# Kernel tuning notes

Measured on AMD Instinct MI355X. Metric: run time of the kernel, lower is better.

## Reference

```python
import jax, jax.numpy as jnp
import numpy as np

H, KV, D, HID = 16, 4, 64, 1024
OUT_MIN, OUT_MAX = 32, 8192  # output_size_max = config.max_position_embeddings


def _score_attn(x, Wq, Wk, Wv, Wo):
    # Full (non-causal, unmasked) GQA attention whose o_proj maps to 1 scalar/token.
    B, S, _ = x.shape
    q = (x @ Wq).reshape(B, S, H, D)
    k = jnp.repeat((x @ Wk).reshape(B, S, KV, D), H // KV, axis=2)  # repeat_kv
    v = jnp.repeat((x @ Wv).reshape(B, S, KV, D), H // KV, axis=2)
    scores = jnp.einsum('bqhd,bkhd->bhqk', q, k) / jnp.asarray(np.sqrt(D), x.dtype)
    a = jax.nn.softmax(scores, axis=-1)
    o = jnp.einsum('bhqk,bkhd->bqhd', a, v).reshape(B, S, H * D)
    return o @ Wo  # (B, S, 1)


def _dynamic_sizes(x, Wq, Wk, Wv, Wo, scale):
    s = _score_attn(x, Wq, Wk, Wv, Wo)               # (B,S,1)
    means = jax.nn.sigmoid(s).mean(axis=1)            # (B,1) (no attention_mask)
    sizes = means.squeeze(-1) * scale * (OUT_MAX - OUT_MIN) + OUT_MIN
    return sizes.astype(jnp.int32)                    # torch .int() truncation


def _segment_ids(sizes_np, S, max_len):
    # torch.linspace(0, L, sz+1).long() boundaries; token t -> segment i with
    # intervals[i] <= t < intervals[i+1]; right-aligned into [max_len] per batch.
    B = len(sizes_np)
    seg = np.zeros((B, S), np.int32)
    t = np.arange(S)
    for b, sz in enumerate(sizes_np):
        sz = int(sz)
        bnd = np.floor(np.linspace(0.0, S, sz + 1, dtype=np.float64)).astype(np.int64)
        s = np.clip(np.searchsorted(bnd, t, side='right') - 1, 0, sz - 1)
        seg[b] = b * max_len + (max_len - sz) + s
    return jnp.asarray(seg)


def setup_inputs() -> dict:
    key = jax.random.key(0)
    ks = jax.random.split(key, 10)
    B, S = 4, 2048
    x = jax.random.normal(ks[0], (B, S, HID), jnp.float32)
    def lin(k, i, o):
        return jax.random.normal(k, (i, o), jnp.float32) / np.sqrt(i).astype(np.float32)
    return dict(
        hidden_states=x,
        Wq1=lin(ks[1], HID, H * D), Wk1=lin(ks[2], HID, KV * D),
        Wv1=lin(ks[3], HID, KV * D), Wo1=lin(ks[4], H * D, 1),
        Wq2=lin(ks[5], HID, H * D), Wk2=lin(ks[6], HID, KV * D),
        Wv2=lin(ks[7], HID, KV * D), Wo2=lin(ks[8], H * D, 1),
        scale_param=jnp.asarray(0.01, jnp.float32),
    )


def reference(hidden_states, Wq1, Wk1, Wv1, Wo1, Wq2, Wk2, Wv2, Wo2, scale_param):
    B, S, Hd = hidden_states.shape
    # 1) size-estimation attention -> per-batch dynamic output sizes (data-dependent shape)
    sizes = _dynamic_sizes(hidden_states, Wq1, Wk1, Wv1, Wo1, scale_param)
    sizes_np = np.asarray(jax.device_get(sizes))
    max_len = int(sizes_np.max())
    seg = _segment_ids(sizes_np, S, max_len)          # (B,S) global segment ids
    # 2) weighted-pooling attention -> per-token sigmoid weights
    w = jax.nn.sigmoid(_score_attn(hidden_states, Wq2, Wk2, Wv2, Wo2)).squeeze(-1)  # (B,S)
    # 3) weighted average pooling over dynamic-size segments (vectorized scatter-add)
    num = jax.ops.segment_sum((hidden_states * w[..., None]).reshape(B * S, Hd),
                              seg.reshape(-1), num_segments=B * max_len)
    den = jax.ops.segment_sum(w.reshape(-1), seg.reshape(-1), num_segments=B * max_len)
    pooled = (num / (den[:, None] + 1e-8)).reshape(B, max_len, Hd)
    out_mask = jnp.arange(max_len)[None, :] >= (max_len - sizes)[:, None]
    return pooled, out_mask, sizes
```

## Files before the change

kernel.cpp:

```cpp
#include <hip/hip_runtime.h>
#include <math.h>

#define TB 256

constexpr int B_ = 4, S_ = 2048, HID_ = 1024, H_ = 16, KV_ = 4, D_ = 64;

typedef short sh8 __attribute__((ext_vector_type(8)));
typedef float fl4 __attribute__((ext_vector_type(4)));
typedef unsigned short u16;
typedef unsigned int u32;

__device__ __forceinline__ u16 f2bf(float f) {
  u32 u = __float_as_uint(f);
  u += 0x7fff + ((u >> 16) & 1);
  return (u16)(u >> 16);
}
__device__ __forceinline__ float bf2f(u16 h) { return __uint_as_float(((u32)h) << 16); }

constexpr size_t XSZ   = (size_t)B_ * S_ * HID_;
constexpr size_t WQH_O = 2 * XSZ;
constexpr size_t WQSZ  = (size_t)2 * HID_ * (H_ * D_);
constexpr size_t WQL_O = WQH_O + WQSZ;
constexpr size_t WKH_O = WQH_O + 2 * WQSZ;
constexpr size_t WKSZ  = (size_t)2 * HID_ * (KV_ * D_);
constexpr size_t WKL_O = WKH_O + WKSZ;
constexpr size_t KH_O  = WKH_O + 2 * WKSZ;
constexpr size_t KSZ   = (size_t)2 * B_ * KV_ * S_ * D_;
constexpr size_t KL_O  = KH_O + KSZ;
constexpr size_t KPLANE = (size_t)S_ * D_;
constexpr size_t FBASE   = (KH_O + 2 * KSZ) / 2;
constexpr size_t U_OFF   = FBASE;
constexpr size_t U_SZ    = (size_t)2 * B_ * H_ * S_;
constexpr size_t WVO_OFF = U_OFF + U_SZ;
constexpr size_t WVO_SZ  = (size_t)HID_ * 32;
constexpr size_t SH_OFF  = WVO_OFF + WVO_SZ;
constexpr size_t SH_SZ   = (size_t)2 * B_ * S_ * H_;
constexpr size_t W_OFF   = SH_OFF + SH_SZ;
constexpr size_t W_SZ    = (size_t)B_ * S_;
constexpr size_t SUM_OFF = W_OFF + W_SZ;

__device__ __forceinline__ void conv_w_body(
    const float* __restrict__ W1, const float* __restrict__ W2,
    u16* __restrict__ OH, u16* __restrict__ OL, int ncols,
    int blk, int tid, float wt[32][257]) {
  int ngrp = ncols >> 8;
  int a = blk / (32 * ngrp);
  int rem = blk - a * 32 * ngrp;
  int cs = rem / ngrp, ng = rem - cs * ngrp;
  const float* W = a ? W2 : W1;
#pragma unroll
  for (int i = 0; i < 8; ++i) {
    int e = tid + i * 256;
    int r = e >> 6, c4 = (e & 63) * 4;
    float4 v = *reinterpret_cast<const float4*>(
        W + ((size_t)(cs * 32 + r)) * ncols + ng * 256 + c4);
    wt[r][c4] = v.x; wt[r][c4 + 1] = v.y; wt[r][c4 + 2] = v.z; wt[r][c4 + 3] = v.w;
  }
  __syncthreads();
  int w = tid >> 6, lane = tid & 63, quad = lane >> 4, col = lane & 15;
  int NF = ncols >> 4;
#pragma unroll
  for (int f = 0; f < 4; ++f) {
    int n16 = w * 4 + f;
    sh8 hh, ll;
#pragma unroll
    for (int j = 0; j < 8; ++j) {
      float v = wt[quad * 8 + j][n16 * 16 + col];
      u16 hb = f2bf(v);
      hh[j] = (short)hb;
      ll[j] = (short)f2bf(v - bf2f(hb));
    }
    size_t fb = (((size_t)a * 32 + cs) * NF + ng * 16 + n16) * 512 + (size_t)lane * 8;
    *reinterpret_cast<sh8*>(OH + fb) = hh;
    *reinterpret_cast<sh8*>(OL + fb) = ll;
  }
}

__global__ __launch_bounds__(TB) void prep1_kernel(
    const float* __restrict__ x,
    const float* __restrict__ Wq1, const float* __restrict__ Wq2,
    const float* __restrict__ Wk1, const float* __restrict__ Wk2,
    const float* __restrict__ Wv1, const float* __restrict__ Wo1,
    const float* __restrict__ Wv2, const float* __restrict__ Wo2,
    float* __restrict__ ws) {
  __shared__ float wt[32][257];
  int blk = blockIdx.x, tid = threadIdx.x;
  u16* wsu = (u16*)ws;
  if (blk < 512) {
    u16* XH = wsu;
    u16* XL = XH + XSZ;
    int bt = blk;
    int w = tid >> 6, lane = tid & 63, quad = lane >> 4, col = lane & 15;
    int b = bt >> 7, t16 = bt & 127;
    const float* row = x + ((size_t)b * S_ + t16 * 16 + col) * HID_;
#pragma unroll
    for (int i = 0; i < 8; ++i) {
      int cs = w + i * 4;
      const float* src = row + cs * 32 + quad * 8;
      float4 v0 = *reinterpret_cast<const float4*>(src);
      float4 v1 = *reinterpret_cast<const float4*>(src + 4);
      float vv[8] = {v0.x, v0.y, v0.z, v0.w, v1.x, v1.y, v1.z, v1.w};
      sh8 hh, ll;
#pragma unroll
      for (int j = 0; j < 8; ++j) {
        u16 hb = f2bf(vv[j]);
        hh[j] = (short)hb;
        ll[j] = (short)f2bf(vv[j] - bf2f(hb));
      }
      size_t fb = ((size_t)bt * 32 + cs) * 512 + (size_t)lane * 8;
      *reinterpret_cast<sh8*>(XH + fb) = hh;
      *reinterpret_cast<sh8*>(XL + fb) = ll;
    }
  } else if (blk < 768) {
    conv_w_body(Wq1, Wq2, wsu + WQH_O, wsu + WQL_O, H_ * D_, blk - 512, tid, wt);
  } else if (blk < 832) {
    conv_w_body(Wk1, Wk2, wsu + WKH_O, wsu + WKL_O, KV_ * D_, blk - 768, tid, wt);
  } else {
    int n = blk - 832, a = n >> 4, h = n & 15, kv = h >> 2;
    const float* Wv = a ? Wv2 : Wv1;
    const float* Wo = a ? Wo2 : Wo1;
    for (int c = tid; c < HID_; c += TB) {
      const float* vr = Wv + (size_t)c * (KV_ * D_) + kv * D_;
      const float* wo = Wo + h * D_;
      float acc = 0.f;
#pragma unroll 16
      for (int d = 0; d < D_; ++d) acc += vr[d] * wo[d];
      ws[WVO_OFF + (size_t)c * 32 + n] = acc;
    }
  }
}

__global__ __launch_bounds__(TB) void prep2_kernel(
    const float* __restrict__ x, float* __restrict__ ws) {
  __shared__ __align__(16) float xs[64][68];
  __shared__ float uw[64][36];
  int blk = blockIdx.x, tid = threadIdx.x;
  if (blk < 1024) {
    int k0 = (blk & 31) * 64;
    int kv = (blk >> 5) & 3;
    int ab = blk >> 7, a = ab >> 2, b = ab & 3;
    int w = tid >> 6, lane = tid & 63, quad = lane >> 4, col = lane & 15;
    const u16* XH = (const u16*)ws;
    const u16* XL = XH + XSZ;
    const u16* WKH = XH + WKH_O;
    const u16* WKL = XH + WKL_O;
    int tq = (w & 1) * 2, nq = (w >> 1) * 2;
    fl4 C[2][2] = {};
#pragma unroll 2
    for (int cs = 0; cs < 32; ++cs) {
      sh8 ah[2], al[2], bh[2], bl[2];
#pragma unroll
      for (int ti = 0; ti < 2; ++ti) {
        size_t fb = (((size_t)b * 128 + (k0 >> 4) + tq + ti) * 32 + cs) * 512 + (size_t)lane * 8;
        ah[ti] = *reinterpret_cast<const sh8*>(XH + fb);
        if (a == 0) al[ti] = *reinterpret_cast<const sh8*>(XL + fb);
      }
#pragma unroll
      for (int ni = 0; ni < 2; ++ni) {
        size_t fb = (((size_t)a * 32 + cs) * 16 + kv * 4 + nq + ni) * 512 + (size_t)lane * 8;
        bh[ni] = *reinterpret_cast<const sh8*>(WKH + fb);
        if (a == 0) bl[ni] = *reinterpret_cast<const sh8*>(WKL + fb);
      }
#pragma unroll
      for (int ti = 0; ti < 2; ++ti)
#pragma unroll
        for (int ni = 0; ni < 2; ++ni) {
          C[ti][ni] = __builtin_amdgcn_mfma_f32_16x16x32_bf16(ah[ti], bh[ni], C[ti][ni], 0, 0, 0);
          if (a == 0) {
            C[ti][ni] = __builtin_amdgcn_mfma_f32_16x16x32_bf16(al[ti], bh[ni], C[ti][ni], 0, 0, 0);
            C[ti][ni] = __builtin_amdgcn_mfma_f32_16x16x32_bf16(ah[ti], bl[ni], C[ti][ni], 0, 0, 0);
          }
        }
    }
#pragma unroll
    for (int ti = 0; ti < 2; ++ti)
#pragma unroll
      for (int ni = 0; ni < 2; ++ni)
#pragma unroll
        for (int r = 0; r < 4; ++r)
          xs[(tq + ti) * 16 + quad * 4 + r][(nq + ni) * 16 + col] = C[ti][ni][r];
    __syncthreads();
    u16* KH = (u16*)ws + KH_O;
    u16* KL = (u16*)ws + KL_O;
    size_t plane = (size_t)((a * B_ + b) * KV_ + kv) * KPLANE;
#pragma unroll
    for (int t = 0; t < 2; ++t) {
      int f = w + t * 4;
      int k16 = f & 3, ds = f >> 2;
      const float* row = &xs[k16 * 16 + col][ds * 32 + quad * 8];
      sh8 hh, ll;
#pragma unroll
      for (int j = 0; j < 8; ++j) {
        float v = row[j];
        u16 hb = f2bf(v);
        hh[j] = (short)hb;
        ll[j] = (short)f2bf(v - bf2f(hb));
      }
      size_t fb = plane + ((size_t)(((k0 >> 4) + k16) * 2 + ds)) * 512 + (size_t)lane * 8;
      *reinterpret_cast<sh8*>(KH + fb) = hh;
      if (a == 0) *reinterpret_cast<sh8*>(KL + fb) = ll;
    }
  } else {
    int i = blk - 1024;
    int k0 = (i & 31) * 64, b = i >> 5;
    int tk = tid >> 2, ng = tid & 3;
    int lr = tid >> 4, lc4 = (tid & 15) * 4;
    float acc[8] = {};
    for (int c0 = 0; c0 < HID_; c0 += 64) {
      __syncthreads();
#pragma unroll
      for (int p = 0; p < 4; ++p) {
        int r = lr + p * 16;
        *reinterpret_cast<float4*>(&xs[r][lc4]) =
            *reinterpret_cast<const float4*>(x + ((size_t)(b * S_ + k0 + r) * HID_ + c0 + lc4));
      }
      {
        int cc = tid >> 3, n4 = (tid & 7) * 4;
        *reinterpret_cast<float4*>(&uw[cc][n4]) =
            *reinterpret_cast<const float4*>(ws + WVO_OFF + (size_t)(c0 + cc) * 32 + n4);
        *reinterpret_cast<float4*>(&uw[cc + 32][n4]) =
            *reinterpret_cast<const float4*>(ws + WVO_OFF + (size_t)(c0 + cc + 32) * 32 + n4);
      }
      __syncthreads();
#pragma unroll 8
      for (int cc = 0; cc < 64; ++cc) {
        float xv = xs[tk][cc];
        float4 a0 = *reinterpret_cast<const float4*>(&uw[cc][ng * 8]);
        float4 a1 = *reinterpret_cast<const float4*>(&uw[cc][ng * 8 + 4]);
        acc[0] += xv * a0.x; acc[1] += xv * a0.y; acc[2] += xv * a0.z; acc[3] += xv * a0.w;
        acc[4] += xv * a1.x; acc[5] += xv * a1.y; acc[6] += xv * a1.z; acc[7] += xv * a1.w;
      }
    }
#pragma unroll
    for (int j = 0; j < 8; ++j) {
      int n = ng * 8 + j, a = n >> 4, h = n & 15;
      ws[U_OFF + ((size_t)(a * B_ + b) * H_ + h) * S_ + k0 + tk] = acc[j];
    }
  }
}

__global__ __launch_bounds__(TB) void attn_kernel(float* __restrict__ ws) {
  __shared__ __align__(16) char smem[64 * 68 * 4];
  float (*Qt)[68] = reinterpret_cast<float(*)[68]>(smem);
  u16* kbuf = reinterpret_cast<u16*>(smem);
  int q0 = blockIdx.x * 64;
  int ah = blockIdx.y, a = ah >> 4, h = ah & 15, kv = h >> 2;
  int b = blockIdx.z;
  int tid = threadIdx.x, w = tid >> 6, lane = tid & 63, quad = lane >> 4, col = lane & 15;
  const u16* XH = (const u16*)ws;
  const u16* XL = XH + XSZ;
  const u16* WQH = XH + WQH_O;
  const u16* WQL = XH + WQL_O;

  {
    int tq = (w & 1) * 2, nq = (w >> 1) * 2;
    fl4 C[2][2] = {};
#pragma unroll 2
    for (int cs = 0; cs < 32; ++cs) {
      sh8 ah_[2], al_[2], bh_[2], bl_[2];
#pragma unroll
      for (int ti = 0; ti < 2; ++ti) {
        size_t fb = (((size_t)b * 128 + (q0 >> 4) + tq + ti) * 32 + cs) * 512 + (size_t)lane * 8;
        ah_[ti] = *reinterpret_cast<const sh8*>(XH + fb);
        if (a == 0) al_[ti] = *reinterpret_cast<const sh8*>(XL + fb);
      }
#pragma unroll
      for (int ni = 0; ni < 2; ++ni) {
        size_t fb = (((size_t)a * 32 + cs) * 64 + h * 4 + nq + ni) * 512 + (size_t)lane * 8;
        bh_[ni] = *reinterpret_cast<const sh8*>(WQH + fb);
        if (a == 0) bl_[ni] = *reinterpret_cast<const sh8*>(WQL + fb);
      }
#pragma unroll
      for (int ti = 0; ti < 2; ++ti)
#pragma unroll
        for (int ni = 0; ni < 2; ++ni) {
          C[ti][ni] = __builtin_amdgcn_mfma_f32_16x16x32_bf16(ah_[ti], bh_[ni], C[ti][ni], 0, 0, 0);
          if (a == 0) {
            C[ti][ni] = __builtin_amdgcn_mfma_f32_16x16x32_bf16(al_[ti], bh_[ni], C[ti][ni], 0, 0, 0);
            C[ti][ni] = __builtin_amdgcn_mfma_f32_16x16x32_bf16(ah_[ti], bl_[ni], C[ti][ni], 0, 0, 0);
          }
        }
    }
#pragma unroll
    for (int ti = 0; ti < 2; ++ti)
#pragma unroll
      for (int ni = 0; ni < 2; ++ni)
#pragma unroll
        for (int r = 0; r < 4; ++r)
          Qt[(nq + ni) * 16 + col][(tq + ti) * 16 + quad * 4 + r] = C[ti][ni][r];
  }
  __syncthreads();

  sh8 qh[2], ql[2];
#pragma unroll
  for (int ds = 0; ds < 2; ++ds)
#pragma unroll
    for (int j = 0; j < 8; ++j) {
      float v = Qt[ds * 32 + quad * 8 + j][w * 16 + col];
      u16 hb = f2bf(v);
      qh[ds][j] = (short)hb;
      if (a == 0) ql[ds][j] = (short)f2bf(v - bf2f(hb));
    }

  const u16* KHg = (const u16*)ws + KH_O + (size_t)((a * B_ + b) * KV_ + kv) * KPLANE;
  const u16* KLg = (const u16*)ws + KL_O + (size_t)((a * B_ + b) * KV_ + kv) * KPLANE;
  int nld = (a == 0) ? 4 : 2;
  const u16* srcp[4];
#pragma unroll
  for (int i = 0; i < 4; ++i) {
    if (i < nld) {
      int c = tid + TB * i, f = c >> 6, ln = c & 63;
      if (a == 0) {
        int st = f >> 2, ds = (f >> 1) & 1, p = f & 1;
        srcp[i] = (p ? KLg : KHg) + ((size_t)(st * 2 + ds)) * 512 + (size_t)ln * 8;
      } else {
        int st = f >> 1, ds = f & 1;
        srcp[i] = KHg + ((size_t)(st * 2 + ds)) * 512 + (size_t)ln * 8;
      }
    }
  }
  const float* up = ws + U_OFF + ((size_t)(a * B_ + b) * H_ + h) * S_ + col;
  float num[4] = {}, den[4] = {};
  for (int kt = 0; kt < 32; ++kt) {
    __syncthreads();
#pragma unroll
    for (int i = 0; i < 4; ++i)
      if (i < nld) {
        *reinterpret_cast<uint4*>(kbuf + (size_t)(tid + TB * i) * 8) =
            *reinterpret_cast<const uint4*>(srcp[i]);
        srcp[i] += 4096;
      }
    __syncthreads();
    float u0 = up[0], u1 = up[16], u2 = up[32], u3 = up[48];
    up += 64;
    float uv[4] = {u0, u1, u2, u3};
    const sh8* kb = (const sh8*)kbuf;
#pragma unroll
    for (int st = 0; st < 4; ++st) {
      sh8 bh0, bh1, bl0, bl1;
      if (a == 0) {
        bh0 = kb[(st * 4 + 0) * 64 + lane];
        bl0 = kb[(st * 4 + 1) * 64 + lane];
        bh1 = kb[(st * 4 + 2) * 64 + lane];
        bl1 = kb[(st * 4 + 3) * 64 + lane];
      } else {
        bh0 = kb[(st * 2 + 0) * 64 + lane];
        bh1 = kb[(st * 2 + 1) * 64 + lane];
      }
      fl4 C = {0.f, 0.f, 0.f, 0.f};
      C = __builtin_amdgcn_mfma_f32_16x16x32_bf16(qh[0], bh0, C, 0, 0, 0);
      C = __builtin_amdgcn_mfma_f32_16x16x32_bf16(qh[1], bh1, C, 0, 0, 0);
      if (a == 0) {
        C = __builtin_amdgcn_mfma_f32_16x16x32_bf16(ql[0], bh0, C, 0, 0, 0);
        C = __builtin_amdgcn_mfma_f32_16x16x32_bf16(ql[1], bh1, C, 0, 0, 0);
        C = __builtin_amdgcn_mfma_f32_16x16x32_bf16(qh[0], bl0, C, 0, 0, 0);
        C = __builtin_amdgcn_mfma_f32_16x16x32_bf16(qh[1], bl1, C, 0, 0, 0);
      }
#pragma unroll
      for (int r = 0; r < 4; ++r) {
        float e = __expf(C[r] * 0.125f);
        den[r] += e;
        num[r] += e * uv[st];
      }
    }
  }
#pragma unroll
  for (int off = 1; off < 16; off <<= 1)
#pragma unroll
    for (int r = 0; r < 4; ++r) {
      den[r] += __shfl_xor(den[r], off);
      num[r] += __shfl_xor(num[r], off);
    }
  if (col == 0) {
#pragma unroll
    for (int r = 0; r < 4; ++r) {
      int q = q0 + w * 16 + quad * 4 + r;
      ws[SH_OFF + ((size_t)(a * B_ + b) * S_ + q) * H_ + h] = num[r] / den[r];
    }
  }
}

__global__ __launch_bounds__(TB) void post_kernel(float* __restrict__ ws) {
  int g = blockIdx.x * TB + threadIdx.x;
  int b = g >> 11, q = g & (S_ - 1);
  const float* sh = ws + SH_OFF;
  float s1 = 0.f, s2 = 0.f;
#pragma unroll
  for (int h = 0; h < H_; ++h) {
    s1 += sh[((size_t)b * S_ + q) * H_ + h];
    s2 += sh[((size_t)(B_ + b) * S_ + q) * H_ + h];
  }
  ws[W_OFF + g] = 1.f / (1.f + expf(-s2));
  double sig = 1.0 / (1.0 + exp(-(double)s1));
#pragma unroll
  for (int off = 1; off < 64; off <<= 1) sig += __shfl_xor(sig, off);
  __shared__ double red[4];
  int tid = threadIdx.x;
  if ((tid & 63) == 0) red[tid >> 6] = sig;
  __syncthreads();
  if (tid == 0)
    atomicAdd(reinterpret_cast<double*>(ws + SUM_OFF) + b,
              red[0] + red[1] + red[2] + red[3]);
}

__global__ __launch_bounds__(TB) void pool_kernel(
    const float* __restrict__ x, const float* __restrict__ scale_p,
    const float* __restrict__ ws, float* __restrict__ out, int max_len) {
  int p = blockIdx.x, b = blockIdx.y;
  double m = reinterpret_cast<const double*>(ws + SUM_OFF)[b] / (double)S_;
  double v = m * (double)(*scale_p) * (double)(8192 - 32) + 32.0;
  int sz = (int)v;
  int s = p - (max_len - sz);
  int tid = threadIdx.x;
  size_t obase = ((size_t)b * max_len + p) * HID_;
  size_t maskbase = (size_t)B_ * max_len * HID_;
  size_t sizebase = maskbase + (size_t)B_ * max_len;
  if (p == 0 && tid == 0) out[sizebase + b] = (float)sz;
  if (s < 0) {
    *reinterpret_cast<float4*>(out + obase + tid * 4) = make_float4(0.f, 0.f, 0.f, 0.f);
    if (tid == 0) out[maskbase + (size_t)b * max_len + p] = 0.f;
    return;
  }
  double step = (double)S_ / (double)sz;
  int t0 = (int)floor((double)s * step);
  int t1 = (s + 1 == sz) ? S_ : (int)floor((double)(s + 1) * step);
  const float* wv = ws + W_OFF + (size_t)b * S_;
  const float* xb = x + (size_t)b * S_ * HID_;
  float den = 0.f, acc0 = 0.f, acc1 = 0.f, acc2 = 0.f, acc3 = 0.f;
  for (int t = t0; t < t1; ++t) {
    float wt = wv[t];
    den += wt;
    float4 xv = *reinterpret_cast<const float4*>(xb + (size_t)t * HID_ + tid * 4);
    acc0 += xv.x * wt; acc1 += xv.y * wt; acc2 += xv.z * wt; acc3 += xv.w * wt;
  }
  float d = den + 1e-8f;
  *reinterpret_cast<float4*>(out + obase + tid * 4) =
      make_float4(acc0 / d, acc1 / d, acc2 / d, acc3 / d);
  if (tid == 0) out[maskbase + (size_t)b * max_len + p] = 1.f;
}

extern "C" void kernel_launch(void* const* d_in, const int* in_sizes, int n_in,
                              void* d_out, int out_size, void* d_ws, size_t ws_size,
                              hipStream_t stream) {
  const float* x    = (const float*)d_in[0];
  const float* Wq1  = (const float*)d_in[1];
  const float* Wk1  = (const float*)d_in[2];
  const float* Wv1  = (const float*)d_in[3];
  const float* Wo1  = (const float*)d_in[4];
  const float* Wq2  = (const float*)d_in[5];
  const float* Wk2  = (const float*)d_in[6];
  const float* Wv2  = (const float*)d_in[7];
  const float* Wo2  = (const float*)d_in[8];
  const float* scale = (const float*)d_in[9];
  float* ws  = (float*)d_ws;
  float* out = (float*)d_out;

  int max_len = (out_size - B_) / (B_ * (HID_ + 1));

  hipMemsetAsync((void*)(ws + SUM_OFF), 0, 4 * sizeof(double), stream);
  prep1_kernel<<<864, TB, 0, stream>>>(x, Wq1, Wq2, Wk1, Wk2, Wv1, Wo1, Wv2, Wo2, ws);
  prep2_kernel<<<1152, TB, 0, stream>>>(x, ws);
  attn_kernel<<<dim3(S_ / 64, 32, B_), TB, 0, stream>>>(ws);
  post_kernel<<<(B_ * S_) / TB, TB, 0, stream>>>(ws);
  pool_kernel<<<dim3(max_len, B_), TB, 0, stream>>>(x, scale, ws, out, max_len);
}
```

Before: 499.9 us.

## Process two query heads per attention block sharing K tiles, prefetch K via registers

Each attention block now handles two heads that share one KV head. Each K tile is loaded once and reused for both heads' score MFMAs, which halves the grid and the K traffic. The next K tile is prefetched into registers while the current one is being computed, giving software pipelining. The hipMemsetAsync is replaced by zeroing inside prep1, which removes one launch. The cost is more registers per thread and serial computation of the two Q projections inside each block.

```diff
diff --git a/kernel.cpp b/kernel.cpp
--- a/kernel.cpp
+++ b/kernel.cpp
@@ -117,6 +117,7 @@
     conv_w_body(Wk1, Wk2, wsu + WKH_O, wsu + WKL_O, KV_ * D_, blk - 768, tid, wt);
   } else {
     int n = blk - 832, a = n >> 4, h = n & 15, kv = h >> 2;
+    if (n == 0 && tid < 8) ws[SUM_OFF + tid] = 0.f;
     const float* Wv = a ? Wv2 : Wv1;
     const float* Wo = a ? Wo2 : Wo1;
     for (int c = tid; c < HID_; c += TB) {
@@ -244,7 +245,8 @@
   float (*Qt)[68] = reinterpret_cast<float(*)[68]>(smem);
   u16* kbuf = reinterpret_cast<u16*>(smem);
   int q0 = blockIdx.x * 64;
-  int ah = blockIdx.y, a = ah >> 4, h = ah & 15, kv = h >> 2;
+  int ah = blockIdx.y, a = ah >> 3, hp = ah & 7;
+  int h0 = hp * 2, kv = hp >> 1;
   int b = blockIdx.z;
   int tid = threadIdx.x, w = tid >> 6, lane = tid & 63, quad = lane >> 4, col = lane & 15;
   const u16* XH = (const u16*)ws;
@@ -252,7 +254,10 @@
   const u16* WQH = XH + WQH_O;
   const u16* WQL = XH + WQL_O;
 
-  {
+  sh8 qh[2][2], ql[2][2];
+#pragma unroll
+  for (int e = 0; e < 2; ++e) {
+    int h = h0 + e;
     int tq = (w & 1) * 2, nq = (w >> 1) * 2;
     fl4 C[2][2] = {};
 #pragma unroll 2
@@ -281,6 +286,7 @@
           }
         }
     }
+    __syncthreads();
 #pragma unroll
     for (int ti = 0; ti < 2; ++ti)
 #pragma unroll
@@ -288,19 +294,17 @@
 #pragma unroll
         for (int r = 0; r < 4; ++r)
           Qt[(nq + ni) * 16 + col][(tq + ti) * 16 + quad * 4 + r] = C[ti][ni][r];
-  }
-  __syncthreads();
-
-  sh8 qh[2], ql[2];
-#pragma unroll
-  for (int ds = 0; ds < 2; ++ds)
-#pragma unroll
-    for (int j = 0; j < 8; ++j) {
-      float v = Qt[ds * 32 + quad * 8 + j][w * 16 + col];
-      u16 hb = f2bf(v);
-      qh[ds][j] = (short)hb;
-      if (a == 0) ql[ds][j] = (short)f2bf(v - bf2f(hb));
-    }
+    __syncthreads();
+#pragma unroll
+    for (int ds = 0; ds < 2; ++ds)
+#pragma unroll
+      for (int j = 0; j < 8; ++j) {
+        float v = Qt[ds * 32 + quad * 8 + j][w * 16 + col];
+        u16 hb = f2bf(v);
+        qh[e][ds][j] = (short)hb;
+        if (a == 0) ql[e][ds][j] = (short)f2bf(v - bf2f(hb));
+      }
+  }
 
   const u16* KHg = (const u16*)ws + KH_O + (size_t)((a * B_ + b) * KV_ + kv) * KPLANE;
   const u16* KLg = (const u16*)ws + KL_O + (size_t)((a * B_ + b) * KV_ + kv) * KPLANE;
@@ -319,21 +323,35 @@
       }
     }
   }
-  const float* up = ws + U_OFF + ((size_t)(a * B_ + b) * H_ + h) * S_ + col;
-  float num[4] = {}, den[4] = {};
+  uint4 rg[4];
+#pragma unroll
+  for (int i = 0; i < 4; ++i)
+    if (i < nld) {
+      rg[i] = *reinterpret_cast<const uint4*>(srcp[i]);
+      srcp[i] += 4096;
+    }
+  const float* up0 = ws + U_OFF + ((size_t)(a * B_ + b) * H_ + h0) * S_ + col;
+  const float* up1 = up0 + S_;
+  float num[2][4] = {}, den[2][4] = {};
   for (int kt = 0; kt < 32; ++kt) {
     __syncthreads();
 #pragma unroll
     for (int i = 0; i < 4; ++i)
-      if (i < nld) {
-        *reinterpret_cast<uint4*>(kbuf + (size_t)(tid + TB * i) * 8) =
-            *reinterpret_cast<const uint4*>(srcp[i]);
-        srcp[i] += 4096;
-      }
+      if (i < nld)
+        *reinterpret_cast<uint4*>(kbuf + (size_t)(tid + TB * i) * 8) = rg[i];
     __syncthreads();
-    float u0 = up[0], u1 = up[16], u2 = up[32], u3 = up[48];
-    up += 64;
-    float uv[4] = {u0, u1, u2, u3};
+    if (kt < 31) {
+#pragma unroll
+      for (int i = 0; i < 4; ++i)
+        if (i < nld) {
+          rg[i] = *reinterpret_cast<const uint4*>(srcp[i]);
+          srcp[i] += 4096;
+        }
+    }
+    float uv[2][4];
+#pragma unroll
+    for (int st = 0; st < 4; ++st) { uv[0][st] = up0[st * 16]; uv[1][st] = up1[st * 16]; }
+    up0 += 64; up1 += 64;
     const sh8* kb = (const sh8*)kbuf;
 #pragma unroll
     for (int st = 0; st < 4; ++st) {
@@ -347,36 +365,43 @@
         bh0 = kb[(st * 2 + 0) * 64 + lane];
         bh1 = kb[(st * 2 + 1) * 64 + lane];
       }
-      fl4 C = {0.f, 0.f, 0.f, 0.f};
-      C = __builtin_amdgcn_mfma_f32_16x16x32_bf16(qh[0], bh0, C, 0, 0, 0);
-      C = __builtin_amdgcn_mfma_f32_16x16x32_bf16(qh[1], bh1, C, 0, 0, 0);
-      if (a == 0) {
-        C = __builtin_amdgcn_mfma_f32_16x16x32_bf16(ql[0], bh0, C, 0, 0, 0);
-        C = __builtin_amdgcn_mfma_f32_16x16x32_bf16(ql[1], bh1, C, 0, 0, 0);
-        C = __builtin_amdgcn_mfma_f32_16x16x32_bf16(qh[0], bl0, C, 0, 0, 0);
-        C = __builtin_amdgcn_mfma_f32_16x16x32_bf16(qh[1], bl1, C, 0, 0, 0);
-      }
+#pragma unroll
+      for (int e = 0; e < 2; ++e) {
+        fl4 C = {0.f, 0.f, 0.f, 0.f};
+        C = __builtin_amdgcn_mfma_f32_16x16x32_bf16(qh[e][0], bh0, C, 0, 0, 0);
+        C = __builtin_amdgcn_mfma_f32_16x16x32_bf16(qh[e][1], bh1, C, 0, 0, 0);
+        if (a == 0) {
+          C = __builtin_amdgcn_mfma_f32_16x16x32_bf16(ql[e][0], bh0, C, 0, 0, 0);
+          C = __builtin_amdgcn_mfma_f32_16x16x32_bf16(ql[e][1], bh1, C, 0, 0, 0);
+          C = __builtin_amdgcn_mfma_f32_16x16x32_bf16(qh[e][0], bl0, C, 0, 0, 0);
+          C = __builtin_amdgcn_mfma_f32_16x16x32_bf16(qh[e][1], bl1, C, 0, 0, 0);
+        }
+#pragma unroll
+        for (int r = 0; r < 4; ++r) {
+          float ex = __expf(C[r] * 0.125f);
+          den[e][r] += ex;
+          num[e][r] += ex * uv[e][st];
+        }
+      }
+    }
+  }
+#pragma unroll
+  for (int off = 1; off < 16; off <<= 1)
+#pragma unroll
+    for (int e = 0; e < 2; ++e)
 #pragma unroll
       for (int r = 0; r < 4; ++r) {
-        float e = __expf(C[r] * 0.125f);
-        den[r] += e;
-        num[r] += e * uv[st];
-      }
-    }
-  }
-#pragma unroll
-  for (int off = 1; off < 16; off <<= 1)
-#pragma unroll
-    for (int r = 0; r < 4; ++r) {
-      den[r] += __shfl_xor(den[r], off);
-      num[r] += __shfl_xor(num[r], off);
-    }
+        den[e][r] += __shfl_xor(den[e][r], off);
+        num[e][r] += __shfl_xor(num[e][r], off);
+      }
   if (col == 0) {
 #pragma unroll
-    for (int r = 0; r < 4; ++r) {
-      int q = q0 + w * 16 + quad * 4 + r;
-      ws[SH_OFF + ((size_t)(a * B_ + b) * S_ + q) * H_ + h] = num[r] / den[r];
-    }
+    for (int e = 0; e < 2; ++e)
+#pragma unroll
+      for (int r = 0; r < 4; ++r) {
+        int q = q0 + w * 16 + quad * 4 + r;
+        ws[SH_OFF + ((size_t)(a * B_ + b) * S_ + q) * H_ + h0 + e] = num[e][r] / den[e][r];
+      }
   }
 }
 
@@ -457,10 +482,9 @@
 
   int max_len = (out_size - B_) / (B_ * (HID_ + 1));
 
-  hipMemsetAsync((void*)(ws + SUM_OFF), 0, 4 * sizeof(double), stream);
   prep1_kernel<<<864, TB, 0, stream>>>(x, Wq1, Wq2, Wk1, Wk2, Wv1, Wo1, Wv2, Wo2, ws);
   prep2_kernel<<<1152, TB, 0, stream>>>(x, ws);
-  attn_kernel<<<dim3(S_ / 64, 32, B_), TB, 0, stream>>>(ws);
+  attn_kernel<<<dim3(S_ / 64, 16, B_), TB, 0, stream>>>(ws);
   post_kernel<<<(B_ * S_) / TB, TB, 0, stream>>>(ws);
   pool_kernel<<<dim3(max_len, B_), TB, 0, stream>>>(x, scale, ws, out, max_len);
 }
```

New measurement: 583.1 us. 1.17x slower.
